# Kernel tuning notes

Measured on AMD Instinct MI355X. Metric: run time of the kernel, lower is better.

The kernel has to match this reference:

```python
import jax, jax.numpy as jnp
import numpy as np

IN_CH, HID, OUT_CH, HEADS = 55, 128, 49, 4
D = HID * HEADS  # 512
N_NODES, N_EDGES = 20000, 320000
NEG_SLOPE = 0.2


def setup_inputs() -> dict:
    key = jax.random.key(0)
    ks = jax.random.split(key, 16)
    s = lambda *sh: 1.0 / np.sqrt(sh[0])
    x = jax.random.normal(ks[0], (N_NODES, IN_CH), dtype=jnp.float32)
    edge_index = jax.random.randint(ks[1], (2, N_EDGES), 0, N_NODES, dtype=jnp.int64)
    p = {
        'x': x,
        'edge_index': edge_index,
        # conv1 (GATv2: lin_l for source, lin_r for target, per-head att vector, out bias)
        'w1_l': jax.random.normal(ks[2], (IN_CH, D), jnp.float32) * s(IN_CH),
        'b1_l': jnp.zeros((D,), jnp.float32),
        'w1_r': jax.random.normal(ks[3], (IN_CH, D), jnp.float32) * s(IN_CH),
        'b1_r': jnp.zeros((D,), jnp.float32),
        'att1': jax.random.normal(ks[4], (HEADS, HID), jnp.float32) * s(HID),
        'bias1': jnp.zeros((D,), jnp.float32),
        # conv2
        'w2_l': jax.random.normal(ks[5], (D, D), jnp.float32) * s(D),
        'b2_l': jnp.zeros((D,), jnp.float32),
        'w2_r': jax.random.normal(ks[6], (D, D), jnp.float32) * s(D),
        'b2_r': jnp.zeros((D,), jnp.float32),
        'att2': jax.random.normal(ks[7], (HEADS, HID), jnp.float32) * s(HID),
        'bias2': jnp.zeros((D,), jnp.float32),
        # classifier
        'w_cls': jax.random.normal(ks[8], (D, OUT_CH), jnp.float32) * s(D),
        'b_cls': jnp.zeros((OUT_CH,), jnp.float32),
    }
    return p


def _gatv2(x, src, dst, n, wl, bl, wr, br, att, bias):
    # GATv2Conv, concat=True. messages flow src -> dst, softmax over dst neighborhoods.
    xl = (x @ wl + bl).reshape(n, HEADS, HID)  # source transform
    xr = (x @ wr + br).reshape(n, HEADS, HID)  # target transform
    e = jax.nn.leaky_relu(xl[src] + xr[dst], NEG_SLOPE)      # [E, H, C]
    score = jnp.einsum('ehc,hc->eh', e, att)                  # [E, H]
    m = jax.ops.segment_max(score, dst, num_segments=n)       # stable softmax per target
    alpha = jnp.exp(score - m[dst])
    denom = jax.ops.segment_sum(alpha, dst, num_segments=n)
    alpha = alpha / denom[dst]
    out = jax.ops.segment_sum(xl[src] * alpha[..., None], dst, num_segments=n)
    return out.reshape(n, D) + bias


def reference(x, edge_index, w1_l, b1_l, w1_r, b1_r, att1, bias1,
              w2_l, b2_l, w2_r, b2_r, att2, bias2, w_cls, b_cls):
    n = x.shape[0]
    # PyG GATv2Conv default add_self_loops=True
    loops = jnp.arange(n, dtype=edge_index.dtype)
    src = jnp.concatenate([edge_index[0], loops])
    dst = jnp.concatenate([edge_index[1], loops])
    h = _gatv2(x, src, dst, n, w1_l, b1_l, w1_r, b1_r, att1, bias1)
    h = jax.nn.elu(h)
    # dropout p=0.5 is identity at eval time
    h = _gatv2(h, src, dst, n, w2_l, b2_l, w2_r, b2_r, att2, bias2)
    h = jax.nn.elu(h)
    return h @ w_cls + b_cls
```

## Files before the change

kernel.cpp:

```cpp
#include <hip/hip_runtime.h>
#include <hip/hip_bf16.h>
#include <float.h>
#include <math.h>

#define N_NODES 20000
#define N_EDGES 320000
#define ET      (N_EDGES + N_NODES)
#define ETB     ((ET + 255) / 256)
#define NPB     ((N_NODES + 255) / 256)
#define DCH     512
#define D2      1024
#define INCH    55
#define INCHP   64
#define OUTCH   49
#define OUTCHP  128
#define NB      130

typedef _Float16 f16;
typedef _Float16 f16x2 __attribute__((ext_vector_type(2)));
typedef _Float16 f16x4 __attribute__((ext_vector_type(4)));
typedef _Float16 f16x8 __attribute__((ext_vector_type(8)));
typedef float    f32x4 __attribute__((ext_vector_type(4)));

#define GPTR(p) ((const __attribute__((address_space(1))) void*)(p))
#define LPTR(p) ((__attribute__((address_space(3))) void*)(p))

__device__ __forceinline__ void transpose_tile(const float* __restrict__ w, f16* __restrict__ o,
                                               int K, int N, int Kp, int bx, int by, int t,
                                               f16 (*tile)[66]) {
    int k0 = by * 64, n0 = bx * 64;
    #pragma unroll
    for (int r = 0; r < 16; ++r) {
        int kl = (t >> 6) + r * 4, nl = t & 63;
        int gk = k0 + kl, gn = n0 + nl;
        tile[kl][nl] = (gk < K && gn < N) ? (f16)w[(size_t)gk * N + gn] : (f16)0.f;
    }
    __syncthreads();
    #pragma unroll
    for (int r = 0; r < 16; ++r) {
        int kl = t & 63, nl = (t >> 6) + r * 4;
        o[(size_t)(n0 + nl) * Kp + k0 + kl] = tile[kl][nl];
    }
}

__global__ __launch_bounds__(256) void prep_all(const float* __restrict__ x, f16* __restrict__ x_h,
                                                const float* __restrict__ w1l, const float* __restrict__ w1r,
                                                const float* __restrict__ w2l, const float* __restrict__ w2r,
                                                const float* __restrict__ wc,
                                                f16* __restrict__ w1T, f16* __restrict__ w2T,
                                                f16* __restrict__ wcT,
                                                int* __restrict__ zeroA,
                                                int* __restrict__ bcur) {
    __shared__ f16 tile[64][66];
    int b = blockIdx.x, t = threadIdx.x;
    if (b < 157) {
        int i = b * 256 + t;
        if (i < 40000) zeroA[i] = 0;
        else if (i < 40000 + NB) bcur[i - 40000] = 0;
        return;
    }
    b -= 157;
    if (b < 5000) {
        int i = b * 256 + t;
        int r = i >> 6, c = i & 63;
        x_h[i] = (c < INCH) ? (f16)x[r * INCH + c] : (f16)0.f;
        return;
    }
    b -= 5000;
    if (b < 8)  { transpose_tile(w1l, w1T, INCH, DCH, INCHP, b, 0, t, tile); return; }
    b -= 8;
    if (b < 8)  { transpose_tile(w1r, w1T + (size_t)DCH * INCHP, INCH, DCH, INCHP, b, 0, t, tile); return; }
    b -= 8;
    if (b < 64) { transpose_tile(w2l, w2T, DCH, DCH, DCH, b & 7, b >> 3, t, tile); return; }
    b -= 64;
    if (b < 64) { transpose_tile(w2r, w2T + (size_t)DCH * DCH, DCH, DCH, DCH, b & 7, b >> 3, t, tile); return; }
    b -= 64;
    transpose_tile(wc, wcT, DCH, OUTCH, DCH, b & 1, b >> 1, t, tile);
}

__global__ void count_kernel(const int* __restrict__ ei, int* __restrict__ counts) {
    int e = blockIdx.x * blockDim.x + threadIdx.x;
    if (e >= ET) return;
    int d = (e < N_EDGES) ? ei[N_EDGES + e] : (e - N_EDGES);
    atomicAdd(&counts[d], 1);
}

__global__ void scan_kernel(const int* __restrict__ counts, int* __restrict__ row_ptr,
                            int* __restrict__ bbase) {
    __shared__ int sdata[1024];
    __shared__ int bh[NB];
    int t = threadIdx.x;
    if (t < NB) bh[t] = 0;
    __syncthreads();
    int per = (N_NODES + 1023) / 1024;
    int b = t * per, e = min(N_NODES, b + per);
    int sum = 0;
    for (int i = b; i < e; ++i) {
        int c = counts[i];
        sum += c;
        atomicAdd(&bh[min(c, NB - 1)], 1);
    }
    sdata[t] = sum;
    __syncthreads();
    for (int off = 1; off < 1024; off <<= 1) {
        int v = (t >= off) ? sdata[t - off] : 0;
        __syncthreads();
        sdata[t] += v;
        __syncthreads();
    }
    int run = (t == 0) ? 0 : sdata[t - 1];
    if (t == 0) row_ptr[0] = 0;
    for (int i = b; i < e; ++i) { run += counts[i]; row_ptr[i + 1] = run; }
    __syncthreads();
    if (t == 0) {
        int acc = 0;
        for (int j = NB - 1; j >= 0; --j) { bbase[j] = acc; acc += bh[j]; }
    }
}

__global__ __launch_bounds__(256) void fill_perm_kernel(const int* __restrict__ ei,
                                                        const int* __restrict__ row_ptr,
                                                        const int* __restrict__ counts,
                                                        const int* __restrict__ bbase,
                                                        int* __restrict__ cursor,
                                                        int* __restrict__ bcur,
                                                        int* __restrict__ esrc,
                                                        int* __restrict__ perm) {
    int blk = blockIdx.x;
    if (blk < ETB) {
        int e = blk * 256 + threadIdx.x;
        if (e >= ET) return;
        int s, d;
        if (e < N_EDGES) { s = ei[e]; d = ei[N_EDGES + e]; }
        else             { s = d = e - N_EDGES; }
        int pos = row_ptr[d] + atomicAdd(&cursor[d], 1);
        esrc[pos] = s;
        return;
    }
    blk -= ETB;
    __shared__ int hist[NB], basep[NB];
    int t = threadIdx.x;
    for (int i = t; i < NB; i += 256) hist[i] = 0;
    __syncthreads();
    int n = blk * 256 + t;
    bool valid = n < N_NODES;
    int bkt = 0, rl = 0;
    if (valid) {
        bkt = min(counts[n], NB - 1);
        rl = atomicAdd(&hist[bkt], 1);
    }
    __syncthreads();
    for (int i = t; i < NB; i += 256)
        if (hist[i] > 0) basep[i] = atomicAdd(&bcur[i], hist[i]);
    __syncthreads();
    if (valid) perm[bbase[bkt] + basep[bkt] + rl] = n;
}

template<int OUT_F16, int DUAL>
__global__ __launch_bounds__(256) void gemm_f16(const f16* __restrict__ A,
                                                const f16* __restrict__ BT,
                                                const float* __restrict__ bl,
                                                const float* __restrict__ br,
                                                void* __restrict__ Cout,
                                                int M, int Ka, int Nv, int ldc) {
    __shared__ __align__(16) f16 As[128][64];
    __shared__ __align__(16) f16 Bs[128][64];
    const int tid = threadIdx.x;
    const int w = tid >> 6, lane = tid & 63;
    int nbx = gridDim.x;
    int nwg = nbx * gridDim.y;
    int bid = blockIdx.y * nbx + blockIdx.x;
    if ((nwg & 7) == 0) bid = (bid & 7) * (nwg >> 3) + (bid >> 3);
    const int m0 = (bid / nbx) * 128, n0 = (bid % nbx) * 128;
    const int wr = (w >> 1) * 64, wc = (w & 1) * 64;
    const int lrow = lane & 15, lk = lane >> 4;
    const int sw = lrow & 7;

    f32x4 acc[4][4] = {};

    for (int k0 = 0; k0 < Ka; k0 += 64) {
        #pragma unroll
        for (int i = 0; i < 4; ++i) {
            int idx = tid + 256 * i;
            int row = idx >> 3;
            int cg  = (idx & 7) ^ (row & 7);
            int gm = m0 + row; gm = gm < M ? gm : M - 1;
            const f16* gp = A + (size_t)gm * Ka + k0 + cg * 8;
            f16* lp = &As[0][0] + (size_t)(w * 64 + 256 * i) * 8;
            __builtin_amdgcn_global_load_lds(GPTR(gp), LPTR(lp), 16, 0, 0);
        }
        #pragma unroll
        for (int i = 0; i < 4; ++i) {
            int idx = tid + 256 * i;
            int row = idx >> 3;
            int cg  = (idx & 7) ^ (row & 7);
            const f16* gp = BT + (size_t)(n0 + row) * Ka + k0 + cg * 8;
            f16* lp = &Bs[0][0] + (size_t)(w * 64 + 256 * i) * 8;
            __builtin_amdgcn_global_load_lds(GPTR(gp), LPTR(lp), 16, 0, 0);
        }
        __syncthreads();
        #pragma unroll
        for (int kk = 0; kk < 64; kk += 32) {
            f16x8 af[4], bf[4];
            #pragma unroll
            for (int m = 0; m < 4; ++m)
                af[m] = *(const f16x8*)&As[wr + m * 16 + lrow][(((kk >> 3) + lk) ^ sw) * 8];
            #pragma unroll
            for (int n = 0; n < 4; ++n)
                bf[n] = *(const f16x8*)&Bs[wc + n * 16 + lrow][(((kk >> 3) + lk) ^ sw) * 8];
            #pragma unroll
            for (int m = 0; m < 4; ++m)
                #pragma unroll
                for (int n = 0; n < 4; ++n)
                    acc[m][n] = __builtin_amdgcn_mfma_f32_16x16x32_f16(bf[n], af[m], acc[m][n], 0, 0, 0);
        }
        __syncthreads();
    }

    const int om = lane & 15, on4 = (lane >> 4) * 4;
    #pragma unroll
    for (int nn = 0; nn < 4; ++nn) {
        int gn0 = n0 + wc + nn * 16 + on4;
        if (OUT_F16) {
            const float* bp = (DUAL && gn0 >= DCH) ? (br + gn0 - DCH) : (bl + gn0);
            float4 bv = *(const float4*)bp;
            float bfr[4] = {bv.x, bv.y, bv.z, bv.w};
            #pragma unroll
            for (int mm = 0; mm < 4; ++mm) {
                int gm = m0 + wr + mm * 16 + om;
                if (gm >= M) continue;
                f16x4 o;
                #pragma unroll
                for (int r = 0; r < 4; ++r) o[r] = (f16)(acc[mm][nn][r] + bfr[r]);
                *(f16x4*)((f16*)Cout + (size_t)gm * ldc + gn0) = o;
            }
        } else {
            #pragma unroll
            for (int mm = 0; mm < 4; ++mm) {
                int gm = m0 + wr + mm * 16 + om;
                if (gm >= M) continue;
                #pragma unroll
                for (int r = 0; r < 4; ++r) {
                    int gn = gn0 + r;
                    if (gn < Nv) ((float*)Cout)[(size_t)gm * ldc + gn] = acc[mm][nn][r] + bl[gn];
                }
            }
        }
    }
}

#define PROC(cc0, cc1, pp)                                                      \
  {                                                                             \
    float sc0 = 0.f, sc1 = 0.f;                                                 \
    _Pragma("unroll")                                                           \
    for (int j = 0; j < 4; ++j) {                                               \
        f16x2 u0 = cc0.q[j] + xr0.q[j];                                         \
        f16x2 u1 = cc1.q[j] + xr1.q[j];                                         \
        f16x2 l0 = __builtin_elementwise_max(u0, u0 * k02);                     \
        f16x2 l1 = __builtin_elementwise_max(u1, u1 * k02);                     \
        sc0 = __builtin_amdgcn_fdot2(l0, at2[j], sc0, false);                   \
        sc1 = __builtin_amdgcn_fdot2(l1, at2[j], sc1, false);                   \
    }                                                                           \
    _Pragma("unroll")                                                           \
    for (int o = 8; o >= 1; o >>= 1) {                                          \
        sc0 += __shfl_xor(sc0, o, 64);                                          \
        sc1 += __shfl_xor(sc1, o, 64);                                          \
    }                                                                           \
    if ((pp) >= deg0) sc0 = -INFINITY;                                          \
    if ((pp) >= deg1) sc1 = -INFINITY;                                          \
    if (__any(sc0 > m0 + 2.f)) {                                                \
        float mn = fmaxf(m0, sc0);                                              \
        f16 fh = (f16)__expf(m0 - mn);                                          \
        f16x2 fh2 = {fh, fh};                                                   \
        d0 *= (float)fh;                                                        \
        _Pragma("unroll") for (int j = 0; j < 4; ++j) acc0.q[j] *= fh2;         \
        m0 = mn;                                                                \
    }                                                                           \
    { f16 wh = (f16)__expf(sc0 - m0); d0 += (float)wh;                          \
      f16x2 wh2 = {wh, wh};                                                     \
      _Pragma("unroll") for (int j = 0; j < 4; ++j)                             \
          acc0.q[j] += wh2 * cc0.q[j]; }                                        \
    if (__any(sc1 > m1 + 2.f)) {                                                \
        float mn = fmaxf(m1, sc1);                                              \
        f16 fh = (f16)__expf(m1 - mn);                                          \
        f16x2 fh2 = {fh, fh};                                                   \
        d1 *= (float)fh;                                                        \
        _Pragma("unroll") for (int j = 0; j < 4; ++j) acc1.q[j] *= fh2;         \
        m1 = mn;                                                                \
    }                                                                           \
    { f16 wh = (f16)__expf(sc1 - m1); d1 += (float)wh;                          \
      f16x2 wh2 = {wh, wh};                                                     \
      _Pragma("unroll") for (int j = 0; j < 4; ++j)                             \
          acc1.q[j] += wh2 * cc1.q[j]; }                                        \
  }

#define LOADU(B0, B1, pp)                                                       \
  {                                                                             \
    int q = (pp) < dcap ? (pp) : dcap - 1;                                      \
    int s0 = __shfl(pre0, q, 64), s1 = __shfl(pre1, q, 64);                     \
    B0.v = *(const f16x8*)(xlr + (size_t)s0 * D2 + lane * 8);                   \
    B1.v = *(const f16x8*)(xlr + (size_t)s1 * D2 + lane * 8);                   \
  }

__global__ __launch_bounds__(256) void edge_agg10(const int* __restrict__ row_ptr,
                                                  const int* __restrict__ esrc,
                                                  const int* __restrict__ perm,
                                                  const f16* __restrict__ xlr,
                                                  const float* __restrict__ att,
                                                  const float* __restrict__ bias,
                                                  f16* __restrict__ out) {
    int wv = (blockIdx.x * 256 + threadIdx.x) >> 6;
    if (wv * 2 >= N_NODES) return;
    int n0 = perm[wv * 2], n1 = perm[wv * 2 + 1];
    int lane = threadIdx.x & 63;

    union U8 { f16x8 v; f16x2 q[4]; };
    U8 xr0, xr1;
    xr0.v = *(const f16x8*)(xlr + (size_t)n0 * D2 + DCH + lane * 8);
    xr1.v = *(const f16x8*)(xlr + (size_t)n1 * D2 + DCH + lane * 8);
    const float4* av = (const float4*)(att + lane * 8);
    float4 a0 = av[0], a1 = av[1];
    f16x2 at2[4] = { f16x2{(f16)a0.x, (f16)a0.y}, f16x2{(f16)a0.z, (f16)a0.w},
                     f16x2{(f16)a1.x, (f16)a1.y}, f16x2{(f16)a1.z, (f16)a1.w} };
    const f16x2 k02 = {(f16)0.2f, (f16)0.2f};

    int beg0 = row_ptr[n0], deg0 = row_ptr[n0 + 1] - beg0;
    int beg1 = row_ptr[n1], deg1 = row_ptr[n1 + 1] - beg1;
    int pre0 = (lane < deg0) ? esrc[beg0 + lane] : 0;
    int pre1 = (lane < deg1) ? esrc[beg1 + lane] : 0;

    U8 acc0, acc1;
    acc0.v = (f16x8)(f16)0.f;
    acc1.v = (f16x8)(f16)0.f;
    float m0 = -FLT_MAX, m1 = -FLT_MAX, d0 = 0.f, d1 = 0.f;

    int dmax = deg0 > deg1 ? deg0 : deg1;
    int dcap = dmax < 64 ? dmax : 64;

    U8 cA0, cA1, cB0, cB1, cC0, cC1, cD0, cD1;
    LOADU(cA0, cA1, 0)
    LOADU(cB0, cB1, 1)
    LOADU(cC0, cC1, 2)
    for (int p = 0; p < dcap; p += 4) {
        LOADU(cD0, cD1, p + 3)
        PROC(cA0, cA1, p)
        if (p + 1 >= dcap) break;
        LOADU(cA0, cA1, p + 4)
        PROC(cB0, cB1, p + 1)
        if (p + 2 >= dcap) break;
        LOADU(cB0, cB1, p + 5)
        PROC(cC0, cC1, p + 2)
        if (p + 3 >= dcap) break;
        LOADU(cC0, cC1, p + 6)
        PROC(cD0, cD1, p + 3)
    }
    for (int p = 64; p < dmax; ++p) {
        int s0 = (p < deg0) ? esrc[beg0 + p] : 0;
        int s1 = (p < deg1) ? esrc[beg1 + p] : 0;
        U8 t0, t1;
        t0.v = *(const f16x8*)(xlr + (size_t)s0 * D2 + lane * 8);
        t1.v = *(const f16x8*)(xlr + (size_t)s1 * D2 + lane * 8);
        PROC(t0, t1, p)
    }

    const float4* bv = (const float4*)(bias + lane * 8);
    float4 b0 = bv[0], b1 = bv[1];
    float bf[8] = {b0.x, b0.y, b0.z, b0.w, b1.x, b1.y, b1.z, b1.w};
    float i0 = 1.f / d0, i1 = 1.f / d1;
    f16x8 o0, o1;
    #pragma unroll
    for (int j = 0; j < 8; ++j) {
        float v0 = (float)acc0.v[j] * i0 + bf[j];
        float v1 = (float)acc1.v[j] * i1 + bf[j];
        v0 = v0 > 0.f ? v0 : __expf(v0) - 1.f;
        v1 = v1 > 0.f ? v1 : __expf(v1) - 1.f;
        o0[j] = (f16)v0;
        o1[j] = (f16)v1;
    }
    *(f16x8*)(out + (size_t)n0 * DCH + lane * 8) = o0;
    *(f16x8*)(out + (size_t)n1 * DCH + lane * 8) = o1;
}

extern "C" void kernel_launch(void* const* d_in, const int* in_sizes, int n_in,
                              void* d_out, int out_size, void* d_ws, size_t ws_size,
                              hipStream_t stream) {
    const float* x     = (const float*)d_in[0];
    const int*   ei    = (const int*)d_in[1];
    const float* w1_l  = (const float*)d_in[2];
    const float* b1_l  = (const float*)d_in[3];
    const float* w1_r  = (const float*)d_in[4];
    const float* b1_r  = (const float*)d_in[5];
    const float* att1  = (const float*)d_in[6];
    const float* bias1 = (const float*)d_in[7];
    const float* w2_l  = (const float*)d_in[8];
    const float* b2_l  = (const float*)d_in[9];
    const float* w2_r  = (const float*)d_in[10];
    const float* b2_r  = (const float*)d_in[11];
    const float* att2  = (const float*)d_in[12];
    const float* bias2 = (const float*)d_in[13];
    const float* wcls  = (const float*)d_in[14];
    const float* bcls  = (const float*)d_in[15];
    float* out = (float*)d_out;

    char* ws = (char*)d_ws;
    f16* x_h = (f16*)ws;
    f16* w1T = x_h + (size_t)N_NODES * INCHP;
    f16* w2T = w1T + (size_t)D2 * INCHP;
    f16* wcT = w2T + (size_t)D2 * DCH;
    f16* xlr = wcT + (size_t)OUTCHP * DCH;
    f16* h   = xlr + (size_t)N_NODES * D2;
    int* row_ptr = (int*)(h + (size_t)N_NODES * DCH);
    int* counts  = row_ptr + (N_NODES + 1);
    int* cursor  = counts + N_NODES;
    int* esrc    = cursor + N_NODES;
    int* perm    = esrc + ET;
    int* bbase   = perm + N_NODES;
    int* bcur    = bbase + NB;

    prep_all<<<5317, 256, 0, stream>>>(x, x_h, w1_l, w1_r, w2_l, w2_r, wcls,
                                       w1T, w2T, wcT, counts, bcur);
    count_kernel<<<(ET + 255) / 256, 256, 0, stream>>>(ei, counts);
    scan_kernel<<<1, 1024, 0, stream>>>(counts, row_ptr, bbase);
    fill_perm_kernel<<<ETB + NPB, 256, 0, stream>>>(ei, row_ptr, counts, bbase,
                                                    cursor, bcur, esrc, perm);

    dim3 blk(256);
    dim3 gD(D2 / 128, (N_NODES + 127) / 128);
    dim3 gC(1, (N_NODES + 127) / 128);
    int eb = (N_NODES / 2 + 3) / 4;

    gemm_f16<1, 1><<<gD, blk, 0, stream>>>(x_h, w1T, b1_l, b1_r, xlr, N_NODES, INCHP, D2, D2);
    edge_agg10<<<eb, blk, 0, stream>>>(row_ptr, esrc, perm, xlr, att1, bias1, h);
    gemm_f16<1, 1><<<gD, blk, 0, stream>>>(h, w2T, b2_l, b2_r, xlr, N_NODES, DCH, D2, D2);
    edge_agg10<<<eb, blk, 0, stream>>>(row_ptr, esrc, perm, xlr, att2, bias2, h);
    gemm_f16<0, 0><<<gC, blk, 0, stream>>>(h, wcT, bcls, bcls, out, N_NODES, DCH, OUTCH, OUTCH);
}
```

Measured before the change: 255.0 us.

## Double-buffer LDS tiles in f16 GEMM to overlap loads with MFMA

The GEMM kernel now keeps two LDS buffers for the A and B tiles. It issues the global-to-LDS loads for the next K tile before running the MFMAs on the current one, and raises wave priority around the MFMA block. This is meant to hide global load latency behind compute instead of stalling at a barrier every K step. In exchange, LDS use doubles to 64KB per block, which may reduce occupancy. The compiler may also insert vmcnt waits before the LDS reads that limit the overlap.

```diff
diff --git a/kernel.cpp b/kernel.cpp
--- a/kernel.cpp
+++ b/kernel.cpp
@@ -163,8 +163,8 @@
                                                 const float* __restrict__ br,
                                                 void* __restrict__ Cout,
                                                 int M, int Ka, int Nv, int ldc) {
-    __shared__ __align__(16) f16 As[128][64];
-    __shared__ __align__(16) f16 Bs[128][64];
+    __shared__ __align__(16) f16 As[2][128][64];
+    __shared__ __align__(16) f16 Bs[2][128][64];
     const int tid = threadIdx.x;
     const int w = tid >> 6, lane = tid & 63;
     int nbx = gridDim.x;
@@ -178,44 +178,56 @@
 
     f32x4 acc[4][4] = {};
 
-    for (int k0 = 0; k0 < Ka; k0 += 64) {
-        #pragma unroll
-        for (int i = 0; i < 4; ++i) {
-            int idx = tid + 256 * i;
-            int row = idx >> 3;
-            int cg  = (idx & 7) ^ (row & 7);
-            int gm = m0 + row; gm = gm < M ? gm : M - 1;
-            const f16* gp = A + (size_t)gm * Ka + k0 + cg * 8;
-            f16* lp = &As[0][0] + (size_t)(w * 64 + 256 * i) * 8;
-            __builtin_amdgcn_global_load_lds(GPTR(gp), LPTR(lp), 16, 0, 0);
-        }
-        #pragma unroll
-        for (int i = 0; i < 4; ++i) {
-            int idx = tid + 256 * i;
-            int row = idx >> 3;
-            int cg  = (idx & 7) ^ (row & 7);
-            const f16* gp = BT + (size_t)(n0 + row) * Ka + k0 + cg * 8;
-            f16* lp = &Bs[0][0] + (size_t)(w * 64 + 256 * i) * 8;
-            __builtin_amdgcn_global_load_lds(GPTR(gp), LPTR(lp), 16, 0, 0);
-        }
-        __syncthreads();
+#define STAGE(BUF, KK0)                                                         \
+    {                                                                           \
+        _Pragma("unroll")                                                       \
+        for (int i = 0; i < 4; ++i) {                                           \
+            int idx = tid + 256 * i;                                            \
+            int row = idx >> 3;                                                 \
+            int cg  = (idx & 7) ^ (row & 7);                                    \
+            int gm = m0 + row; gm = gm < M ? gm : M - 1;                        \
+            const f16* gp = A + (size_t)gm * Ka + (KK0) + cg * 8;               \
+            f16* lp = &As[BUF][0][0] + (size_t)(w * 64 + 256 * i) * 8;          \
+            __builtin_amdgcn_global_load_lds(GPTR(gp), LPTR(lp), 16, 0, 0);     \
+        }                                                                       \
+        _Pragma("unroll")                                                       \
+        for (int i = 0; i < 4; ++i) {                                           \
+            int idx = tid + 256 * i;                                            \
+            int row = idx >> 3;                                                 \
+            int cg  = (idx & 7) ^ (row & 7);                                    \
+            const f16* gp = BT + (size_t)(n0 + row) * Ka + (KK0) + cg * 8;      \
+            f16* lp = &Bs[BUF][0][0] + (size_t)(w * 64 + 256 * i) * 8;          \
+            __builtin_amdgcn_global_load_lds(GPTR(gp), LPTR(lp), 16, 0, 0);     \
+        }                                                                       \
+    }
+
+    const int nt = Ka >> 6;
+    STAGE(0, 0)
+    __syncthreads();
+    int cur = 0;
+    for (int t = 0; t < nt; ++t) {
+        if (t + 1 < nt) STAGE(cur ^ 1, (t + 1) * 64)
+        __builtin_amdgcn_s_setprio(1);
         #pragma unroll
         for (int kk = 0; kk < 64; kk += 32) {
             f16x8 af[4], bf[4];
             #pragma unroll
             for (int m = 0; m < 4; ++m)
-                af[m] = *(const f16x8*)&As[wr + m * 16 + lrow][(((kk >> 3) + lk) ^ sw) * 8];
+                af[m] = *(const f16x8*)&As[cur][wr + m * 16 + lrow][(((kk >> 3) + lk) ^ sw) * 8];
             #pragma unroll
             for (int n = 0; n < 4; ++n)
-                bf[n] = *(const f16x8*)&Bs[wc + n * 16 + lrow][(((kk >> 3) + lk) ^ sw) * 8];
+                bf[n] = *(const f16x8*)&Bs[cur][wc + n * 16 + lrow][(((kk >> 3) + lk) ^ sw) * 8];
             #pragma unroll
             for (int m = 0; m < 4; ++m)
                 #pragma unroll
                 for (int n = 0; n < 4; ++n)
                     acc[m][n] = __builtin_amdgcn_mfma_f32_16x16x32_f16(bf[n], af[m], acc[m][n], 0, 0, 0);
         }
+        __builtin_amdgcn_s_setprio(0);
         __syncthreads();
-    }
+        cur ^= 1;
+    }
+#undef STAGE
 
     const int om = lane & 15, on4 = (lane >> 4) * 4;
     #pragma unroll
```

Measured after the change: 254.2 us. No clear change (-0.3%).

## Fuse CSR build into one cooperative kernel with grid syncs

Applied to the files above, without the earlier changes.

Replaces the count, single-block scan and fill/permutation kernels with one cooperative kernel of 79 blocks. Stages are separated by grid.sync, and the scan becomes a parallel block-level scan followed by a scan of block partials. The aim is to remove two kernel launches and the serial 1024-thread scan. In exchange the edge-count and scatter passes now run on only 79 blocks using grid-stride loops, which may cut their parallelism and add grid barrier cost.

```diff
diff --git a/kernel.cpp b/kernel.cpp
--- a/kernel.cpp
+++ b/kernel.cpp
@@ -1,13 +1,14 @@
 #include <hip/hip_runtime.h>
 #include <hip/hip_bf16.h>
+#include <hip/hip_cooperative_groups.h>
 #include <float.h>
 #include <math.h>
+
+namespace cg = cooperative_groups;
 
 #define N_NODES 20000
 #define N_EDGES 320000
 #define ET      (N_EDGES + N_NODES)
-#define ETB     ((ET + 255) / 256)
-#define NPB     ((N_NODES + 255) / 256)
 #define DCH     512
 #define D2      1024
 #define INCH    55
@@ -15,6 +16,8 @@
 #define OUTCH   49
 #define OUTCHP  128
 #define NB      130
+#define NCB     79
+#define ZINTS   (20000 + 20000 + NB + NB + 128)
 
 typedef _Float16 f16;
 typedef _Float16 f16x2 __attribute__((ext_vector_type(2)));
@@ -49,17 +52,15 @@
                                                 const float* __restrict__ wc,
                                                 f16* __restrict__ w1T, f16* __restrict__ w2T,
                                                 f16* __restrict__ wcT,
-                                                int* __restrict__ zeroA,
-                                                int* __restrict__ bcur) {
+                                                int* __restrict__ zeroA) {
     __shared__ f16 tile[64][66];
     int b = blockIdx.x, t = threadIdx.x;
-    if (b < 157) {
+    if (b < 158) {
         int i = b * 256 + t;
-        if (i < 40000) zeroA[i] = 0;
-        else if (i < 40000 + NB) bcur[i - 40000] = 0;
+        if (i < ZINTS) zeroA[i] = 0;
         return;
     }
-    b -= 157;
+    b -= 158;
     if (b < 5000) {
         int i = b * 256 + t;
         int r = i >> 6, c = i & 63;
@@ -78,82 +79,94 @@
     transpose_tile(wc, wcT, DCH, OUTCH, DCH, b & 1, b >> 1, t, tile);
 }
 
-__global__ void count_kernel(const int* __restrict__ ei, int* __restrict__ counts) {
-    int e = blockIdx.x * blockDim.x + threadIdx.x;
-    if (e >= ET) return;
-    int d = (e < N_EDGES) ? ei[N_EDGES + e] : (e - N_EDGES);
-    atomicAdd(&counts[d], 1);
-}
-
-__global__ void scan_kernel(const int* __restrict__ counts, int* __restrict__ row_ptr,
-                            int* __restrict__ bbase) {
-    __shared__ int sdata[1024];
-    __shared__ int bh[NB];
-    int t = threadIdx.x;
-    if (t < NB) bh[t] = 0;
+__global__ __launch_bounds__(256) void csr_all(const int* __restrict__ ei,
+                                               int* __restrict__ counts,
+                                               int* __restrict__ cursor,
+                                               int* __restrict__ bcur,
+                                               int* __restrict__ gbh,
+                                               int* __restrict__ partial,
+                                               int* __restrict__ row_ptr,
+                                               int* __restrict__ bbase,
+                                               int* __restrict__ esrc,
+                                               int* __restrict__ perm) {
+    cg::grid_group grid = cg::this_grid();
+    __shared__ int sd[256];
+    __shared__ int hist[NB], basep[NB];
+    const int t = threadIdx.x, b = blockIdx.x;
+    const int gt = b * 256 + t;
+    const int GSTRIDE = NCB * 256;
+
+    for (int e = gt; e < ET; e += GSTRIDE) {
+        int d = (e < N_EDGES) ? ei[N_EDGES + e] : (e - N_EDGES);
+        atomicAdd(&counts[d], 1);
+    }
+    grid.sync();
+
+    const int n = gt;
+    const int c = (n < N_NODES) ? counts[n] : 0;
+    if (n < N_NODES) atomicAdd(&gbh[min(c, NB - 1)], 1);
+    sd[t] = c;
     __syncthreads();
-    int per = (N_NODES + 1023) / 1024;
-    int b = t * per, e = min(N_NODES, b + per);
-    int sum = 0;
-    for (int i = b; i < e; ++i) {
-        int c = counts[i];
-        sum += c;
-        atomicAdd(&bh[min(c, NB - 1)], 1);
-    }
-    sdata[t] = sum;
+    for (int off = 1; off < 256; off <<= 1) {
+        int v = (t >= off) ? sd[t - off] : 0;
+        __syncthreads();
+        sd[t] += v;
+        __syncthreads();
+    }
+    const int incl = sd[t];
+    if (t == 255) partial[b] = incl;
+    grid.sync();
+
+    if (b == 0) {
+        int pv = (t < NCB) ? partial[t] : 0;
+        sd[t] = pv;
+        __syncthreads();
+        for (int off = 1; off < 256; off <<= 1) {
+            int v = (t >= off) ? sd[t - off] : 0;
+            __syncthreads();
+            sd[t] += v;
+            __syncthreads();
+        }
+        if (t < NCB) partial[t] = sd[t];
+        __syncthreads();
+        int bv = (t < NB) ? gbh[NB - 1 - t] : 0;
+        sd[t] = bv;
+        __syncthreads();
+        for (int off = 1; off < 256; off <<= 1) {
+            int v = (t >= off) ? sd[t - off] : 0;
+            __syncthreads();
+            sd[t] += v;
+            __syncthreads();
+        }
+        if (t < NB) bbase[NB - 1 - t] = sd[t] - bv;
+    }
+    grid.sync();
+
+    const int boff = (b == 0) ? 0 : partial[b - 1];
+    if (n < N_NODES) row_ptr[n + 1] = boff + incl;
+    if (gt == 0) row_ptr[0] = 0;
+    for (int i = t; i < NB; i += 256) hist[i] = 0;
     __syncthreads();
-    for (int off = 1; off < 1024; off <<= 1) {
-        int v = (t >= off) ? sdata[t - off] : 0;
-        __syncthreads();
-        sdata[t] += v;
-        __syncthreads();
-    }
-    int run = (t == 0) ? 0 : sdata[t - 1];
-    if (t == 0) row_ptr[0] = 0;
-    for (int i = b; i < e; ++i) { run += counts[i]; row_ptr[i + 1] = run; }
+    const bool valid = n < N_NODES;
+    int bkt = 0, rl = 0;
+    if (valid) {
+        bkt = min(c, NB - 1);
+        rl = atomicAdd(&hist[bkt], 1);
+    }
     __syncthreads();
-    if (t == 0) {
-        int acc = 0;
-        for (int j = NB - 1; j >= 0; --j) { bbase[j] = acc; acc += bh[j]; }
-    }
-}
-
-__global__ __launch_bounds__(256) void fill_perm_kernel(const int* __restrict__ ei,
-                                                        const int* __restrict__ row_ptr,
-                                                        const int* __restrict__ counts,
-                                                        const int* __restrict__ bbase,
-                                                        int* __restrict__ cursor,
-                                                        int* __restrict__ bcur,
-                                                        int* __restrict__ esrc,
-                                                        int* __restrict__ perm) {
-    int blk = blockIdx.x;
-    if (blk < ETB) {
-        int e = blk * 256 + threadIdx.x;
-        if (e >= ET) return;
+    for (int i = t; i < NB; i += 256)
+        if (hist[i] > 0) basep[i] = atomicAdd(&bcur[i], hist[i]);
+    __syncthreads();
+    if (valid) perm[bbase[bkt] + basep[bkt] + rl] = n;
+    grid.sync();
+
+    for (int e = gt; e < ET; e += GSTRIDE) {
         int s, d;
         if (e < N_EDGES) { s = ei[e]; d = ei[N_EDGES + e]; }
         else             { s = d = e - N_EDGES; }
         int pos = row_ptr[d] + atomicAdd(&cursor[d], 1);
         esrc[pos] = s;
-        return;
-    }
-    blk -= ETB;
-    __shared__ int hist[NB], basep[NB];
-    int t = threadIdx.x;
-    for (int i = t; i < NB; i += 256) hist[i] = 0;
-    __syncthreads();
-    int n = blk * 256 + t;
-    bool valid = n < N_NODES;
-    int bkt = 0, rl = 0;
-    if (valid) {
-        bkt = min(counts[n], NB - 1);
-        rl = atomicAdd(&hist[bkt], 1);
-    }
-    __syncthreads();
-    for (int i = t; i < NB; i += 256)
-        if (hist[i] > 0) basep[i] = atomicAdd(&bcur[i], hist[i]);
-    __syncthreads();
-    if (valid) perm[bbase[bkt] + basep[bkt] + rl] = n;
+    }
 }
 
 template<int OUT_F16, int DUAL>
@@ -412,17 +425,25 @@
     int* row_ptr = (int*)(h + (size_t)N_NODES * DCH);
     int* counts  = row_ptr + (N_NODES + 1);
     int* cursor  = counts + N_NODES;
-    int* esrc    = cursor + N_NODES;
+    int* bcur    = cursor + N_NODES;
+    int* gbh     = bcur + NB;
+    int* partial = gbh + NB;
+    int* bbase   = partial + 128;
+    int* esrc    = bbase + NB;
     int* perm    = esrc + ET;
-    int* bbase   = perm + N_NODES;
-    int* bcur    = bbase + NB;
-
-    prep_all<<<5317, 256, 0, stream>>>(x, x_h, w1_l, w1_r, w2_l, w2_r, wcls,
-                                       w1T, w2T, wcT, counts, bcur);
-    count_kernel<<<(ET + 255) / 256, 256, 0, stream>>>(ei, counts);
-    scan_kernel<<<1, 1024, 0, stream>>>(counts, row_ptr, bbase);
-    fill_perm_kernel<<<ETB + NPB, 256, 0, stream>>>(ei, row_ptr, counts, bbase,
-                                                    cursor, bcur, esrc, perm);
+
+    prep_all<<<5318, 256, 0, stream>>>(x, x_h, w1_l, w1_r, w2_l, w2_r, wcls,
+                                       w1T, w2T, wcT, counts);
+    {
+        const int* ei_p = ei;
+        int *c_p = counts, *cu_p = cursor, *bc_p = bcur, *gb_p = gbh,
+            *pa_p = partial, *rp_p = row_ptr, *bb_p = bbase, *es_p = esrc, *pm_p = perm;
+        void* args[] = { (void*)&ei_p, (void*)&c_p, (void*)&cu_p, (void*)&bc_p,
+                         (void*)&gb_p, (void*)&pa_p, (void*)&rp_p, (void*)&bb_p,
+                         (void*)&es_p, (void*)&pm_p };
+        hipLaunchCooperativeKernel((const void*)csr_all, dim3(NCB), dim3(256),
+                                   args, 0, stream);
+    }
 
     dim3 blk(256);
     dim3 gD(D2 / 128, (N_NODES + 127) / 128);
```

After: 346.1 us. 35.7% more time.
